# Optimization experiments

Measured on AMD Instinct MI355X. Metric: run time of the kernel, lower is better.

## Reference

```python
import jax, jax.numpy as jnp
import numpy as np

EPS = 1e-5

def _bn(h, gamma, beta):
    # BatchNorm1d in training mode: per-channel stats over the batch dim (L=1)
    m = jnp.mean(h, axis=0)
    v = jnp.var(h, axis=0)  # biased variance, as torch uses for normalization
    return gamma * (h - m) * jax.lax.rsqrt(v + EPS) + beta

def setup_inputs() -> dict:
    key = jax.random.key(0)
    ks = jax.random.split(key, 8)
    vocab, emb = 8192, 512
    inter = (vocab + emb) // 2  # 4352
    N = 8192
    x_t = jax.random.randint(ks[0], (N,), 0, vocab, dtype=jnp.int64)
    W1 = jax.random.normal(ks[1], (inter, vocab), dtype=jnp.float32) * 0.02
    b1 = jax.random.normal(ks[2], (inter,), dtype=jnp.float32) * 0.02
    g1 = jnp.ones((inter,), dtype=jnp.float32)
    beta1 = jnp.zeros((inter,), dtype=jnp.float32)
    W2 = jax.random.normal(ks[3], (emb, inter), dtype=jnp.float32) * 0.02
    b2 = jax.random.normal(ks[4], (emb,), dtype=jnp.float32) * 0.02
    g2 = jnp.ones((emb,), dtype=jnp.float32)
    beta2 = jnp.zeros((emb,), dtype=jnp.float32)
    return {"x_t": x_t, "W1": W1, "b1": b1, "g1": g1, "beta1": beta1,
            "W2": W2, "b2": b2, "g2": g2, "beta2": beta2}

def reference(x_t, W1, b1, g1, beta1, W2, b2, g2, beta2):
    # one_hot(x_t) @ Conv1d(k=1) weight == gather of W1 columns (same math, no dense one-hot)
    h1 = W1.T[x_t] + b1                      # [N, inter]
    h1 = jax.nn.gelu(_bn(h1, g1, beta1), approximate=False)
    h2 = h1 @ W2.T + b2                      # [N, emb]
    out = jax.nn.gelu(_bn(h2, g2, beta2), approximate=False)
    return out
```

## Files before the change

kernel.cpp:

```cpp
#include <hip/hip_runtime.h>
#include <hip/hip_bf16.h>
#include <math.h>

typedef __attribute__((ext_vector_type(8))) short short8;
typedef __attribute__((ext_vector_type(4))) float f32x4;

#define VOCAB 8192
#define NSAMP 8192
#define INTER 4352
#define EMB   512

#define OFF_CNT    0
#define OFF_A1     32768
#define OFF_M1     50176
#define OFF_A2     67584
#define OFF_M2     69632
#define OFF_PS1B   71680
#define OFF_DONE   333824
#define OFF_PS2B   1120256
#define OFF_W2B    2168832
#define OFF_HACT   6625280
#define OFF_H2     77928448

__device__ __forceinline__ float gelu_exact(float x) {
    return 0.5f * x * (1.0f + erff(x * 0.70710678118654752f));
}
__device__ __forceinline__ unsigned short f2bf(float x) {
    __hip_bfloat16 b = __float2bfloat16(x);
    return *reinterpret_cast<unsigned short*>(&b);
}
__device__ __forceinline__ void async16(const unsigned short* g, unsigned short* l) {
    __builtin_amdgcn_global_load_lds(
        (const __attribute__((address_space(1))) void*)g,
        (__attribute__((address_space(3))) void*)l, 16, 0, 0);
}

__global__ __launch_bounds__(1024) void k_hist1b(const int* __restrict__ xt,
                                                 int* __restrict__ cnt,
                                                 unsigned* __restrict__ done) {
    __shared__ int h[VOCAB];
    const int t = threadIdx.x;
    #pragma unroll
    for (int i = 0; i < 8; ++i) h[t + i * 1024] = 0;
    if (t == 0) *done = 0u;
    __syncthreads();
    const int4* x4 = (const int4*)xt;
    int4 a = x4[t], b = x4[t + 1024];
    atomicAdd(&h[a.x], 1); atomicAdd(&h[a.y], 1);
    atomicAdd(&h[a.z], 1); atomicAdd(&h[a.w], 1);
    atomicAdd(&h[b.x], 1); atomicAdd(&h[b.y], 1);
    atomicAdd(&h[b.z], 1); atomicAdd(&h[b.w], 1);
    __syncthreads();
    #pragma unroll
    for (int i = 0; i < 2; ++i)
        ((int4*)cnt)[t + i * 1024] = ((const int4*)h)[t + i * 1024];
}

__global__ __launch_bounds__(256) void k_stats1(const float* __restrict__ W1,
                                                const int* __restrict__ cnt,
                                                const float* __restrict__ g1,
                                                float* __restrict__ a1,
                                                float* __restrict__ m1) {
    const int t = threadIdx.x, lane = t & 63, w = t >> 6;
    const int row = blockIdx.x * 4 + w;
    const float* wr = W1 + (size_t)row * VOCAB;
    float s1 = 0.f, s2 = 0.f;
    #pragma unroll 8
    for (int it = 0; it < 32; ++it) {
        int v = it * 256 + lane * 4;
        float4 x = *(const float4*)(wr + v);
        int4 c = *(const int4*)(cnt + v);
        float cx = (float)c.x, cy = (float)c.y, cz = (float)c.z, cw = (float)c.w;
        s1 += cx * x.x + cy * x.y + cz * x.z + cw * x.w;
        s2 += cx * x.x * x.x + cy * x.y * x.y + cz * x.z * x.z + cw * x.w * x.w;
    }
    #pragma unroll
    for (int d = 1; d < 64; d <<= 1) {
        s1 += __shfl_xor(s1, d);
        s2 += __shfl_xor(s2, d);
    }
    if (lane == 0) {
        float m = s1 * (1.f / NSAMP);
        float var = s2 * (1.f / NSAMP) - m * m;
        a1[row] = g1[row] * rsqrtf(var + 1e-5f);
        m1[row] = m;
    }
}

__global__ __launch_bounds__(256) void k_buildw2(const float* __restrict__ W1,
                                                 const float* __restrict__ a1,
                                                 const float* __restrict__ m1,
                                                 const float* __restrict__ beta1,
                                                 unsigned short* __restrict__ Hact,
                                                 const float* __restrict__ W2,
                                                 unsigned short* __restrict__ W2b) {
    const int bx = blockIdx.x;
    const int t = threadIdx.x;
    if (bx >= 2176) {
        int idx = ((bx - 2176) * 256 + t) * 4;
        float4 w = *(const float4*)(W2 + idx);
        ushort4 u;
        u.x = f2bf(w.x); u.y = f2bf(w.y); u.z = f2bf(w.z); u.w = f2bf(w.w);
        *(ushort4*)(W2b + idx) = u;
        return;
    }
    const int i0 = (bx % 68) * 64;
    const int v0 = (bx / 68) * 256;
    const int c0 = (t & 15) * 4;
    const int vg = (t >> 4) * 4;
    float4 av = *(const float4*)(a1 + i0 + c0);
    float4 mv = *(const float4*)(m1 + i0 + c0);
    float4 bv = *(const float4*)(beta1 + i0 + c0);
    const float* ap = (const float*)&av;
    const float* mp = (const float*)&mv;
    const float* bp = (const float*)&bv;
    #pragma unroll
    for (int vi = 0; vi < 4; ++vi) {
        int vb = v0 + vi * 64 + vg;
        float wf[4][4];
        #pragma unroll
        for (int j = 0; j < 4; ++j)
            *(float4*)&wf[j][0] = *(const float4*)(W1 + (size_t)(i0 + c0 + j) * VOCAB + vb);
        #pragma unroll
        for (int k = 0; k < 4; ++k) {
            ushort4 o;
            o.x = f2bf(gelu_exact(ap[0] * (wf[0][k] - mp[0]) + bp[0]));
            o.y = f2bf(gelu_exact(ap[1] * (wf[1][k] - mp[1]) + bp[1]));
            o.z = f2bf(gelu_exact(ap[2] * (wf[2][k] - mp[2]) + bp[2]));
            o.w = f2bf(gelu_exact(ap[3] * (wf[3][k] - mp[3]) + bp[3]));
            *(ushort4*)&Hact[(size_t)(vb + k) * INTER + i0 + c0] = o;
        }
    }
}

__global__ __launch_bounds__(512) void k_gemm(const unsigned short* __restrict__ A,
                                              const unsigned short* __restrict__ B,
                                              const int* __restrict__ cnt,
                                              float* __restrict__ h2,
                                              float* __restrict__ ps1,
                                              float* __restrict__ ps2,
                                              const float* __restrict__ g2,
                                              float* __restrict__ a2,
                                              float* __restrict__ m2,
                                              unsigned* __restrict__ done) {
    __shared__ __align__(16) unsigned short sA[4][128 * 64];
    __shared__ __align__(16) unsigned short sB[4][128 * 64];
    const int bid = blockIdx.x;
    const int mblk = bid & 63;
    const int nblk = bid >> 6;
    const int m0 = mblk * 128;
    const int n0 = nblk * 128;
    const int t = threadIdx.x;
    const int lane = t & 63;
    const int wave = t >> 6;
    const int wr = wave >> 2, wc = wave & 3;
    const int mq = lane & 15, kq = lane >> 4;
    const int srow = lane >> 3;
    const int sgrp = lane & 7;
    const int scol = (sgrp ^ srow) * 8;
    const int swz = mq & 7;

    const unsigned short* Ab = A + (size_t)(m0 + wave * 16 + srow) * INTER + scol;
    const unsigned short* Bb = B + (size_t)(n0 + wave * 16 + srow) * INTER + scol;

    f32x4 acc[4][2];
    #pragma unroll
    for (int r = 0; r < 4; ++r)
        #pragma unroll
        for (int c = 0; c < 2; ++c) acc[r][c] = (f32x4){0.f, 0.f, 0.f, 0.f};

    auto stage = [&](int buf, int tile) {
        int k0 = tile * 64;
        async16(Ab + k0,                     &sA[buf][(wave * 16) * 64]);
        async16(Ab + (size_t)8 * INTER + k0, &sA[buf][(wave * 16 + 8) * 64]);
        async16(Bb + k0,                     &sB[buf][(wave * 16) * 64]);
        async16(Bb + (size_t)8 * INTER + k0, &sB[buf][(wave * 16 + 8) * 64]);
    };
    auto compute = [&](int buf) {
        #pragma unroll
        for (int kk = 0; kk < 64; kk += 32) {
            const int gbase = kq + (kk >> 3);
            short8 af[4], bfr[2];
            #pragma unroll
            for (int r = 0; r < 4; ++r)
                af[r] = *(const short8*)&sA[buf][(wr * 64 + r * 16 + mq) * 64 + ((gbase ^ swz) * 8)];
            #pragma unroll
            for (int c = 0; c < 2; ++c)
                bfr[c] = *(const short8*)&sB[buf][(wc * 32 + c * 16 + mq) * 64 + ((gbase ^ swz) * 8)];
            __builtin_amdgcn_s_setprio(1);
            #pragma unroll
            for (int r = 0; r < 4; ++r)
                #pragma unroll
                for (int c = 0; c < 2; ++c)
                    acc[r][c] = __builtin_amdgcn_mfma_f32_16x16x32_bf16(af[r], bfr[c], acc[r][c], 0, 0, 0);
            __builtin_amdgcn_s_setprio(0);
        }
    };

#define PSTEP(BUF, VM, STG, TILE3)                                 \
    {                                                              \
        asm volatile("s_waitcnt vmcnt(" #VM ")" ::: "memory");     \
        __builtin_amdgcn_sched_barrier(0);                         \
        __builtin_amdgcn_s_barrier();                              \
        __builtin_amdgcn_sched_barrier(0);                         \
        if (STG) stage(((BUF) + 3) & 3, TILE3);                    \
        compute(BUF);                                              \
    }

    stage(0, 0); stage(1, 1); stage(2, 2);
    #pragma unroll 1
    for (int tt = 0; tt < 64; tt += 4) {
        PSTEP(0, 8, 1, tt + 3)
        PSTEP(1, 8, 1, tt + 4)
        PSTEP(2, 8, 1, tt + 5)
        PSTEP(3, 8, 1, tt + 6)
    }
    PSTEP(0, 8, 1, 67)
    PSTEP(1, 8, 0, 0)
    PSTEP(2, 4, 0, 0)
    PSTEP(3, 0, 0, 0)
#undef PSTEP

    float s1[2] = {0.f, 0.f}, s2[2] = {0.f, 0.f};
    #pragma unroll
    for (int r = 0; r < 4; ++r) {
        const int rowb = m0 + wr * 64 + r * 16 + kq * 4;
        int4 cw = *(const int4*)(cnt + rowb);
        float w0 = (float)cw.x, w1 = (float)cw.y, w2 = (float)cw.z, w3 = (float)cw.w;
        #pragma unroll
        for (int c = 0; c < 2; ++c) {
            const int col = n0 + wc * 32 + c * 16 + mq;
            float v0 = acc[r][c][0], v1 = acc[r][c][1], v2 = acc[r][c][2], v3 = acc[r][c][3];
            h2[(size_t)(rowb + 0) * EMB + col] = v0;
            h2[(size_t)(rowb + 1) * EMB + col] = v1;
            h2[(size_t)(rowb + 2) * EMB + col] = v2;
            h2[(size_t)(rowb + 3) * EMB + col] = v3;
            s1[c] += w0 * v0 + w1 * v1 + w2 * v2 + w3 * v3;
            s2[c] += w0 * v0 * v0 + w1 * v1 * v1 + w2 * v2 * v2 + w3 * v3 * v3;
        }
    }
    #pragma unroll
    for (int c = 0; c < 2; ++c) {
        s1[c] += __shfl_xor(s1[c], 16);
        s2[c] += __shfl_xor(s2[c], 16);
        s1[c] += __shfl_xor(s1[c], 32);
        s2[c] += __shfl_xor(s2[c], 32);
    }
    if (lane < 16) {
        const int slot = mblk * 2 + wr;
        #pragma unroll
        for (int c = 0; c < 2; ++c) {
            const int col = n0 + wc * 32 + c * 16 + mq;
            ps1[(size_t)col * 128 + slot] = s1[c];
            ps2[(size_t)col * 128 + slot] = s2[c];
        }
    }

    __shared__ bool sLast;
    __syncthreads();
    if (t == 0) {
        __threadfence();
        sLast = (atomicAdd(done, 1u) == 255u);
    }
    __syncthreads();
    if (sLast) {
        __threadfence();
        float f1 = 0.f, f2 = 0.f;
        const float4* p1 = (const float4*)(ps1 + (size_t)t * 128);
        const float4* p2 = (const float4*)(ps2 + (size_t)t * 128);
        #pragma unroll 8
        for (int i = 0; i < 32; ++i) {
            float4 u = p1[i]; f1 += u.x + u.y + u.z + u.w;
            float4 v = p2[i]; f2 += v.x + v.y + v.z + v.w;
        }
        float m = f1 * (1.f / NSAMP);
        float var = f2 * (1.f / NSAMP) - m * m;
        a2[t] = g2[t] * rsqrtf(var + 1e-5f);
        m2[t] = m;
    }
}

__global__ __launch_bounds__(256) void k_final(const float* __restrict__ h2,
                                               const int* __restrict__ xt,
                                               const float* __restrict__ a2,
                                               const float* __restrict__ m2,
                                               const float* __restrict__ beta2,
                                               float* __restrict__ out) {
    const int t = threadIdx.x;
    const int n = blockIdx.x * 2 + (t >> 7);
    const int e = (t & 127) * 4;
    const int v = xt[n];
    float4 h = *(const float4*)(h2 + (size_t)v * EMB + e);
    float4 a = *(const float4*)(a2 + e);
    float4 m = *(const float4*)(m2 + e);
    float4 b = *(const float4*)(beta2 + e);
    float4 o;
    o.x = gelu_exact(a.x * (h.x - m.x) + b.x);
    o.y = gelu_exact(a.y * (h.y - m.y) + b.y);
    o.z = gelu_exact(a.z * (h.z - m.z) + b.z);
    o.w = gelu_exact(a.w * (h.w - m.w) + b.w);
    *(float4*)(out + (size_t)n * EMB + e) = o;
}

extern "C" void kernel_launch(void* const* d_in, const int* in_sizes, int n_in,
                              void* d_out, int out_size, void* d_ws, size_t ws_size,
                              hipStream_t stream) {
    const int* xt      = (const int*)d_in[0];
    const float* W1    = (const float*)d_in[1];
    const float* g1    = (const float*)d_in[3];
    const float* beta1 = (const float*)d_in[4];
    const float* W2    = (const float*)d_in[5];
    const float* g2    = (const float*)d_in[7];
    const float* beta2 = (const float*)d_in[8];
    float* out = (float*)d_out;

    char* ws = (char*)d_ws;
    int*   cnt  = (int*)  (ws + OFF_CNT);
    float* a1   = (float*)(ws + OFF_A1);
    float* m1   = (float*)(ws + OFF_M1);
    float* a2   = (float*)(ws + OFF_A2);
    float* m2   = (float*)(ws + OFF_M2);
    float* ps1b = (float*)(ws + OFF_PS1B);
    float* ps2b = (float*)(ws + OFF_PS2B);
    unsigned* done = (unsigned*)(ws + OFF_DONE);
    unsigned short* W2b  = (unsigned short*)(ws + OFF_W2B);
    unsigned short* Hact = (unsigned short*)(ws + OFF_HACT);
    float* h2   = (float*)(ws + OFF_H2);

    k_hist1b<<<1, 1024, 0, stream>>>(xt, cnt, done);
    k_stats1<<<1088, 256, 0, stream>>>(W1, cnt, g1, a1, m1);
    k_buildw2<<<4352, 256, 0, stream>>>(W1, a1, m1, beta1, Hact, W2, W2b);
    k_gemm<<<256, 512, 0, stream>>>(Hact, W2b, cnt, h2, ps1b, ps2b, g2, a2, m2, done);
    k_final<<<4096, 256, 0, stream>>>(h2, xt, a2, m2, beta2, out);
}
```

Measured before the change: 353.8 us.

## Shrink GEMM tile to 128x64 with 256 threads and double buffering

The GEMM now uses 128x64 output tiles with 4 waves per block, launching 512 blocks instead of 256 blocks of 128x128 with 8 waves. The 4-stage async pipeline with explicit vmcnt waits is replaced by a simple 2-buffer loop with __syncthreads, which cuts LDS use per block. The aim is more blocks for better CU occupancy on the 256-CU part. In exchange it gives up operand reuse per tile and the deeper prefetch that hid load latency. The last-block BN2 reduction is adapted to the new block count and covers 512 channels with 256 threads.

```diff
diff --git a/kernel.cpp b/kernel.cpp
--- a/kernel.cpp
+++ b/kernel.cpp
@@ -133,7 +133,7 @@
     }
 }
 
-__global__ __launch_bounds__(512) void k_gemm(const unsigned short* __restrict__ A,
+__global__ __launch_bounds__(256) void k_gemm(const unsigned short* __restrict__ A,
                                               const unsigned short* __restrict__ B,
                                               const int* __restrict__ cnt,
                                               float* __restrict__ h2,
@@ -143,24 +143,24 @@
                                               float* __restrict__ a2,
                                               float* __restrict__ m2,
                                               unsigned* __restrict__ done) {
-    __shared__ __align__(16) unsigned short sA[4][128 * 64];
-    __shared__ __align__(16) unsigned short sB[4][128 * 64];
+    __shared__ __align__(16) unsigned short sA[2][128 * 64];
+    __shared__ __align__(16) unsigned short sB[2][64 * 64];
     const int bid = blockIdx.x;
     const int mblk = bid & 63;
     const int nblk = bid >> 6;
     const int m0 = mblk * 128;
-    const int n0 = nblk * 128;
+    const int n0 = nblk * 64;
     const int t = threadIdx.x;
     const int lane = t & 63;
     const int wave = t >> 6;
-    const int wr = wave >> 2, wc = wave & 3;
+    const int wr = wave >> 1, wc = wave & 1;
     const int mq = lane & 15, kq = lane >> 4;
     const int srow = lane >> 3;
     const int sgrp = lane & 7;
     const int scol = (sgrp ^ srow) * 8;
     const int swz = mq & 7;
 
-    const unsigned short* Ab = A + (size_t)(m0 + wave * 16 + srow) * INTER + scol;
+    const unsigned short* Ab = A + (size_t)(m0 + wave * 32 + srow) * INTER + scol;
     const unsigned short* Bb = B + (size_t)(n0 + wave * 16 + srow) * INTER + scol;
 
     f32x4 acc[4][2];
@@ -170,11 +170,13 @@
         for (int c = 0; c < 2; ++c) acc[r][c] = (f32x4){0.f, 0.f, 0.f, 0.f};
 
     auto stage = [&](int buf, int tile) {
-        int k0 = tile * 64;
-        async16(Ab + k0,                     &sA[buf][(wave * 16) * 64]);
-        async16(Ab + (size_t)8 * INTER + k0, &sA[buf][(wave * 16 + 8) * 64]);
-        async16(Bb + k0,                     &sB[buf][(wave * 16) * 64]);
-        async16(Bb + (size_t)8 * INTER + k0, &sB[buf][(wave * 16 + 8) * 64]);
+        const int k0 = tile * 64;
+        #pragma unroll
+        for (int p = 0; p < 4; ++p)
+            async16(Ab + (size_t)(p * 8) * INTER + k0, &sA[buf][(wave * 32 + p * 8) * 64]);
+        #pragma unroll
+        for (int p = 0; p < 2; ++p)
+            async16(Bb + (size_t)(p * 8) * INTER + k0, &sB[buf][(wave * 16 + p * 8) * 64]);
     };
     auto compute = [&](int buf) {
         #pragma unroll
@@ -197,29 +199,15 @@
         }
     };
 
-#define PSTEP(BUF, VM, STG, TILE3)                                 \
-    {                                                              \
-        asm volatile("s_waitcnt vmcnt(" #VM ")" ::: "memory");     \
-        __builtin_amdgcn_sched_barrier(0);                         \
-        __builtin_amdgcn_s_barrier();                              \
-        __builtin_amdgcn_sched_barrier(0);                         \
-        if (STG) stage(((BUF) + 3) & 3, TILE3);                    \
-        compute(BUF);                                              \
-    }
-
-    stage(0, 0); stage(1, 1); stage(2, 2);
+    stage(0, 0);
+    __syncthreads();
     #pragma unroll 1
-    for (int tt = 0; tt < 64; tt += 4) {
-        PSTEP(0, 8, 1, tt + 3)
-        PSTEP(1, 8, 1, tt + 4)
-        PSTEP(2, 8, 1, tt + 5)
-        PSTEP(3, 8, 1, tt + 6)
-    }
-    PSTEP(0, 8, 1, 67)
-    PSTEP(1, 8, 0, 0)
-    PSTEP(2, 4, 0, 0)
-    PSTEP(3, 0, 0, 0)
-#undef PSTEP
+    for (int ti = 0; ti < 67; ++ti) {
+        stage((ti + 1) & 1, ti + 1);
+        compute(ti & 1);
+        __syncthreads();
+    }
+    compute(1);
 
     float s1[2] = {0.f, 0.f}, s2[2] = {0.f, 0.f};
     #pragma unroll
@@ -260,23 +248,26 @@
     __syncthreads();
     if (t == 0) {
         __threadfence();
-        sLast = (atomicAdd(done, 1u) == 255u);
+        sLast = (atomicAdd(done, 1u) == 511u);
     }
     __syncthreads();
     if (sLast) {
         __threadfence();
-        float f1 = 0.f, f2 = 0.f;
-        const float4* p1 = (const float4*)(ps1 + (size_t)t * 128);
-        const float4* p2 = (const float4*)(ps2 + (size_t)t * 128);
-        #pragma unroll 8
-        for (int i = 0; i < 32; ++i) {
-            float4 u = p1[i]; f1 += u.x + u.y + u.z + u.w;
-            float4 v = p2[i]; f2 += v.x + v.y + v.z + v.w;
-        }
-        float m = f1 * (1.f / NSAMP);
-        float var = f2 * (1.f / NSAMP) - m * m;
-        a2[t] = g2[t] * rsqrtf(var + 1e-5f);
-        m2[t] = m;
+        #pragma unroll
+        for (int e = t; e < 512; e += 256) {
+            float f1 = 0.f, f2 = 0.f;
+            const float4* p1 = (const float4*)(ps1 + (size_t)e * 128);
+            const float4* p2 = (const float4*)(ps2 + (size_t)e * 128);
+            #pragma unroll 8
+            for (int i = 0; i < 32; ++i) {
+                float4 u = p1[i]; f1 += u.x + u.y + u.z + u.w;
+                float4 v = p2[i]; f2 += v.x + v.y + v.z + v.w;
+            }
+            float m = f1 * (1.f / NSAMP);
+            float var = f2 * (1.f / NSAMP) - m * m;
+            a2[e] = g2[e] * rsqrtf(var + 1e-5f);
+            m2[e] = m;
+        }
     }
 }
 
@@ -330,6 +321,6 @@
     k_hist1b<<<1, 1024, 0, stream>>>(xt, cnt, done);
     k_stats1<<<1088, 256, 0, stream>>>(W1, cnt, g1, a1, m1);
     k_buildw2<<<4352, 256, 0, stream>>>(W1, a1, m1, beta1, Hact, W2, W2b);
-    k_gemm<<<256, 512, 0, stream>>>(Hact, W2b, cnt, h2, ps1b, ps2b, g2, a2, m2, done);
+    k_gemm<<<512, 256, 0, stream>>>(Hact, W2b, cnt, h2, ps1b, ps2b, g2, a2, m2, done);
     k_final<<<4096, 256, 0, stream>>>(h2, xt, a2, m2, beta2, out);
 }
```

After: 368.4 us. 1.04x slower.
